# Kernel optimization log

Hardware: AMD Instinct MI355X
Metric: run time of the kernel (lower is better)

Reference implementation:

```python
import jax, jax.numpy as jnp
import numpy as np

B, S, DM1, DM2, DK, DV = 8, 2048, 768, 768, 64, 64
EPS = 1e-5


def setup_inputs() -> dict:
    key = jax.random.key(0)
    ks = jax.random.split(key, 8)
    s1 = 1.0 / np.sqrt(DM1)
    s2 = 1.0 / np.sqrt(DM2)
    return {
        "x_1": jax.random.normal(ks[0], (B, S, DM1), jnp.float32),
        "x_2": jax.random.normal(ks[1], (B, S, DM2), jnp.float32),
        "Wq": jax.random.uniform(ks[2], (DM1, DK), jnp.float32, -s1, s1),
        "bq": jnp.zeros((DK,), jnp.float32),
        "Wk": jax.random.uniform(ks[3], (DM2, DK), jnp.float32, -s2, s2),
        "bk": jnp.zeros((DK,), jnp.float32),
        "Wv": jax.random.uniform(ks[4], (DM2, DV), jnp.float32, -s2, s2),
        "bv": jnp.zeros((DV,), jnp.float32),
        "gamma": jnp.ones((DV,), jnp.float32),
        "beta": jnp.zeros((DV,), jnp.float32),
    }


def reference(x_1, x_2, Wq, bq, Wk, bk, Wv, bv, gamma, beta):
    q = jnp.einsum("bsd,dk->bsk", x_1, Wq) + bq            # [B,S,DK]
    k = jnp.einsum("bsd,dk->bsk", x_2, Wk) + bk            # [B,S,DK]
    v = jnp.einsum("bsd,dv->bsv", x_2, Wv) + bv            # [B,S,DV]
    scores = jnp.einsum("bqk,bsk->bqs", q, k) / jnp.sqrt(jnp.float32(DK))
    w = jax.nn.softmax(scores, axis=-1)                    # [B,S,S]
    # reverse-weight transform (reverse=True)
    dim = w.shape[1]
    w = (1.0 - w) / (dim - 1)
    attn = jnp.einsum("bqs,bsv->bqv", w, v)                # [B,S,DV]
    mu = jnp.mean(attn, axis=-1, keepdims=True)
    var = jnp.var(attn, axis=-1, keepdims=True)
    out = (attn - mu) * jax.lax.rsqrt(var + EPS) * gamma + beta
    return out
```

## Files before the change

### kernel.cpp

```cpp
#include <hip/hip_runtime.h>
#include <hip/hip_bf16.h>

#define BATCH 8
#define SEQ   2048
#define DM    768
#define DD    64
#define BS (BATCH * SEQ)
#define SCALEQ 0.1803369380478f

typedef __bf16 bf16x8 __attribute__((ext_vector_type(8)));
typedef float  f32x4  __attribute__((ext_vector_type(4)));
typedef short  short8 __attribute__((ext_vector_type(8)));
typedef short  short4v __attribute__((ext_vector_type(4)));

#define MFMA16(a, b, c) __builtin_amdgcn_mfma_f32_16x16x32_bf16((a), (b), (c), 0, 0, 0)

__device__ __forceinline__ short f2bf(float x) {
    unsigned u = __builtin_bit_cast(unsigned, x);
    u = (u + 0x7fffu + ((u >> 16) & 1u)) >> 16;
    return (short)u;
}
__device__ __forceinline__ float bf2f(short s) {
    unsigned u = ((unsigned)(unsigned short)s) << 16;
    return __builtin_bit_cast(float, u);
}
__device__ __forceinline__ bf16x8 cvt8(float4 a, float4 b) {
    bf16x8 r;
    r[0] = (__bf16)a.x; r[1] = (__bf16)a.y; r[2] = (__bf16)a.z; r[3] = (__bf16)a.w;
    r[4] = (__bf16)b.x; r[5] = (__bf16)b.y; r[6] = (__bf16)b.z; r[7] = (__bf16)b.w;
    return r;
}

__global__ void prep_w_kernel(const float* __restrict__ Wq, const float* __restrict__ Wk,
                              const float* __restrict__ Wv, short* __restrict__ Wt,
                              float* __restrict__ C) {
    int idx = blockIdx.x * 256 + threadIdx.x;
    if (idx < BATCH * DD) C[idx] = 0.f;
    if (idx >= 3 * DM * DD) return;
    int m = idx / (DM * DD);
    int r = (idx % (DM * DD)) / DD;
    int c = idx % DD;
    const float* W = (m == 0) ? Wq : (m == 1) ? Wk : Wv;
    float scale = (m == 0) ? SCALEQ : 1.0f;
    Wt[m * DM * DD + c * DM + r] = f2bf(W[r * DD + c] * scale);
}

__global__ __launch_bounds__(256, 2) void proj_kernel(
        const float* __restrict__ x1, const float* __restrict__ x2,
        const short* __restrict__ Wt,
        const float* __restrict__ bq, const float* __restrict__ bk,
        const float* __restrict__ bv,
        short* __restrict__ Qs, short* __restrict__ Kb, short* __restrict__ Vtb,
        float* __restrict__ C) {
    const int tid = threadIdx.x, wave = tid >> 6, lane = tid & 63;
    const int quad = lane >> 4, l15 = lane & 15;
    const int typ = blockIdx.x % 3;
    const int g   = blockIdx.x / 3;
    const int r0  = g * 64;
    const float* x = (typ == 0) ? x1 : x2;
    const int col = wave * 16 + l15;

    const short* wp = Wt + ((size_t)typ * DD + col) * DM + quad * 8;
    bf16x8 wreg[24];
#pragma unroll
    for (int st = 0; st < 24; st++)
        wreg[st] = *(const bf16x8*)(wp + st * 32);

    const float* xp = x + (size_t)(r0 + l15) * DM + quad * 8;

    f32x4 acc[4] = {};
    float4 ca[4], cb[4];
#pragma unroll
    for (int rn = 0; rn < 4; rn++) {
        const float* p = xp + (size_t)(rn * 16) * DM;
        ca[rn] = *(const float4*)(p);
        cb[rn] = *(const float4*)(p + 4);
    }
#pragma unroll
    for (int st = 0; st < 24; st++) {
        float4 na[4], nb[4];
        if (st + 1 < 24) {
#pragma unroll
            for (int rn = 0; rn < 4; rn++) {
                const float* p = xp + (size_t)(rn * 16) * DM + (st + 1) * 32;
                na[rn] = *(const float4*)(p);
                nb[rn] = *(const float4*)(p + 4);
            }
        }
#pragma unroll
        for (int rn = 0; rn < 4; rn++) {
            bf16x8 af = cvt8(ca[rn], cb[rn]);
            acc[rn] = MFMA16(af, wreg[st], acc[rn]);
        }
#pragma unroll
        for (int rn = 0; rn < 4; rn++) { ca[rn] = na[rn]; cb[rn] = nb[rn]; }
    }

    if (typ == 0) {
        float bb = bq[col] * SCALEQ;
#pragma unroll
        for (int rn = 0; rn < 4; rn++)
#pragma unroll
            for (int r = 0; r < 4; r++)
                Qs[(size_t)(r0 + rn * 16 + quad * 4 + r) * DD + col] = f2bf(acc[rn][r] + bb);
    } else if (typ == 1) {
        float bb = bk[col];
#pragma unroll
        for (int rn = 0; rn < 4; rn++)
#pragma unroll
            for (int r = 0; r < 4; r++)
                Kb[(size_t)(r0 + rn * 16 + quad * 4 + r) * DD + col] = f2bf(acc[rn][r] + bb);
    } else {
        const int b  = r0 >> 11;
        const int sb = r0 & 2047;
        float bb = bv[col];
        short* vout = Vtb + ((size_t)b * DD + col) * SEQ + sb;
        float cs = 0.f;
#pragma unroll
        for (int rn = 0; rn < 4; rn++) {
            short4v pk;
#pragma unroll
            for (int r = 0; r < 4; r++) {
                pk[r] = f2bf(acc[rn][r] + bb);
                cs += bf2f(pk[r]);
            }
            *(short4v*)(vout + rn * 16 + quad * 4) = pk;
        }
        cs += __shfl_xor(cs, 16);
        cs += __shfl_xor(cs, 32);
        if (quad == 0) atomicAdd(&C[b * DD + col], cs);
    }
}

#define PBS 72
__global__ __launch_bounds__(256, 2) void flash_kernel(
        const short* __restrict__ Q, const short* __restrict__ K,
        const short* __restrict__ Vt,
        short* __restrict__ Yp, float* __restrict__ Dp) {
    __shared__ __align__(16) short pbuf[4][64 * PBS];
    __shared__ float dl[4][64];
    const int tid  = threadIdx.x;
    const int wave = tid >> 6, lane = tid & 63, quad = lane >> 4, l15 = lane & 15;
    const int blk = blockIdx.x;
    const int b = blk & 7, qt = (blk >> 3) & 31, half = blk >> 8;
    const int q0 = qt * 64;

    bf16x8 qf[4][2];
#pragma unroll
    for (int qn = 0; qn < 4; qn++)
#pragma unroll
        for (int kc = 0; kc < 2; kc++)
            qf[qn][kc] = *(const bf16x8*)(Q + ((size_t)(b * SEQ + q0 + qn * 16 + l15)) * DD
                                          + kc * 32 + quad * 8);

    const short* Kbp = K  + (size_t)b * SEQ * DD;
    const short* Vbp = Vt + (size_t)b * DD * SEQ;
    f32x4 y[4][4] = {};
    float den[4] = {0.f, 0.f, 0.f, 0.f};
    short* pw = &pbuf[wave][0];

    const int s_begin = half * 1024 + wave * 256;
    for (int s0 = s_begin; s0 < s_begin + 256; s0 += 64) {
#pragma unroll
        for (int tn = 0; tn < 4; tn++) {
            const short* kf = Kbp + (size_t)(s0 + tn * 16 + l15) * DD + quad * 8;
            bf16x8 ka0 = *(const bf16x8*)kf;
            bf16x8 ka1 = *(const bf16x8*)(kf + 32);
#pragma unroll
            for (int qn = 0; qn < 4; qn++) {
                f32x4 z = {0.f, 0.f, 0.f, 0.f};
                z = MFMA16(ka0, qf[qn][0], z);
                z = MFMA16(ka1, qf[qn][1], z);
                short4v pk;
#pragma unroll
                for (int r = 0; r < 4; r++) {
                    float p = __builtin_amdgcn_exp2f(z[r]);
                    den[qn] += p;
                    pk[r] = f2bf(p);
                }
                *(short4v*)&pw[(qn * 16 + l15) * PBS + tn * 16 + quad * 4] = pk;
            }
        }
#pragma unroll
        for (int kc = 0; kc < 2; kc++) {
            bf16x8 pB[4];
#pragma unroll
            for (int qn = 0; qn < 4; qn++)
                pB[qn] = *(const bf16x8*)&pw[(qn * 16 + l15) * PBS + kc * 32 + quad * 8];
#pragma unroll
            for (int vn = 0; vn < 4; vn++) {
                bf16x8 va = *(const bf16x8*)(Vbp + (size_t)(vn * 16 + l15) * SEQ
                                             + s0 + kc * 32 + quad * 8);
#pragma unroll
                for (int qn = 0; qn < 4; qn++)
                    y[qn][vn] = MFMA16(va, pB[qn], y[qn][vn]);
            }
        }
    }
#pragma unroll
    for (int qn = 0; qn < 4; qn++) {
        den[qn] += __shfl_xor(den[qn], 16);
        den[qn] += __shfl_xor(den[qn], 32);
    }
#pragma unroll
    for (int qn = 0; qn < 4; qn++) {
#pragma unroll
        for (int vn = 0; vn < 4; vn++) {
            short4v pk;
#pragma unroll
            for (int r = 0; r < 4; r++) pk[r] = f2bf(y[qn][vn][r]);
            *(short4v*)&pw[(qn * 16 + l15) * PBS + vn * 16 + quad * 4] = pk;
        }
        if (quad == 0) dl[wave][qn * 16 + l15] = den[qn];
    }
    __syncthreads();
    {
        const int q = wave * 16 + l15;
        float D = dl[0][q] + dl[1][q] + dl[2][q] + dl[3][q];
        float ys[16];
#pragma unroll
        for (int j = 0; j < 16; j++) ys[j] = 0.f;
#pragma unroll
        for (int u = 0; u < 4; u++) {
#pragma unroll
            for (int h = 0; h < 2; h++) {
                bf16x8 t = *(const bf16x8*)&pbuf[u][q * PBS + quad * 16 + h * 8];
#pragma unroll
                for (int j = 0; j < 8; j++) ys[h * 8 + j] += (float)t[j];
            }
        }
        const size_t row = (size_t)b * SEQ + q0 + q;
        short8 o0, o1;
#pragma unroll
        for (int j = 0; j < 8; j++) { o0[j] = f2bf(ys[j]); o1[j] = f2bf(ys[8 + j]); }
        short* yout = Yp + ((size_t)half * BS + row) * DD + quad * 16;
        *(short8*)yout = o0;
        *(short8*)(yout + 8) = o1;
        if (quad == 0) Dp[half * BS + row] = D;
    }
}

__global__ __launch_bounds__(256) void reduce_ln_kernel(
        const short* __restrict__ Yp, const float* __restrict__ Dp,
        const float* __restrict__ C, const float* __restrict__ gamma,
        const float* __restrict__ beta, float* __restrict__ out) {
    const int row = blockIdx.x * 4 + (threadIdx.x >> 6);
    const int v = threadIdx.x & 63;
    const int b = row >> 11;
    float Y = bf2f(Yp[(size_t)row * DD + v]) + bf2f(Yp[((size_t)BS + row) * DD + v]);
    float D = Dp[row] + Dp[BS + row];
    float attn = (C[b * DD + v] - Y / D) * (1.0f / (float)(SEQ - 1));
    float msum = attn, ssum = attn * attn;
#pragma unroll
    for (int m = 1; m < 64; m <<= 1) {
        msum += __shfl_xor(msum, m);
        ssum += __shfl_xor(ssum, m);
    }
    float mu = msum * (1.0f / 64.0f);
    float var = ssum * (1.0f / 64.0f) - mu * mu;
    float rs = rsqrtf(var + 1e-5f);
    out[(size_t)row * DD + v] = (attn - mu) * rs * gamma[v] + beta[v];
}

extern "C" void kernel_launch(void* const* d_in, const int* in_sizes, int n_in,
                              void* d_out, int out_size, void* d_ws, size_t ws_size,
                              hipStream_t stream) {
    const float* x1    = (const float*)d_in[0];
    const float* x2    = (const float*)d_in[1];
    const float* Wq    = (const float*)d_in[2];
    const float* bq    = (const float*)d_in[3];
    const float* Wk    = (const float*)d_in[4];
    const float* bk    = (const float*)d_in[5];
    const float* Wv    = (const float*)d_in[6];
    const float* bv    = (const float*)d_in[7];
    const float* gamma = (const float*)d_in[8];
    const float* beta  = (const float*)d_in[9];
    float* out = (float*)d_out;

    char* ws = (char*)d_ws;
    short* Qs  = (short*)(ws);
    short* Kbf = (short*)(ws + (2ull << 20));
    short* Vtb = (short*)(ws + (4ull << 20));
    short* Wt  = (short*)(ws + (6ull << 20));
    float* Cc  = (float*)(ws + (6ull << 20) + 3 * DM * DD * 2);
    short* Yp  = (short*)(ws + (7ull << 20));
    float* Dp  = (float*)(ws + (11ull << 20));

    prep_w_kernel<<<576, 256, 0, stream>>>(Wq, Wk, Wv, Wt, Cc);
    proj_kernel<<<768, 256, 0, stream>>>(x1, x2, Wt, bq, bk, bv, Qs, Kbf, Vtb, Cc);
    flash_kernel<<<512, 256, 0, stream>>>(Qs, Kbf, Vtb, Yp, Dp);
    reduce_ln_kernel<<<BS / 4, 256, 0, stream>>>(Yp, Dp, Cc, gamma, beta, out);
}
```

Measured before the change: 212.6 us.

## Stage projection weights through double-buffered LDS via global_load_lds

The projection kernel no longer keeps all 24 weight fragments in registers per lane. It streams the weights in four phases into a double-buffered shared-memory tile using direct global-to-LDS loads, and raises the launch bound from 2 to 3 blocks per CU. The aim is to cut register pressure and raise occupancy so the memory-bound streaming of x hides latency better. In exchange it adds LDS reads and a block barrier per phase, and correctness relies on the async LDS loads having completed before each barrier.

Result: slower. 219.5 us (+3.2%).

```diff
diff --git a/kernel.cpp b/kernel.cpp
--- a/kernel.cpp
+++ b/kernel.cpp
@@ -29,6 +29,11 @@
     r[0] = (__bf16)a.x; r[1] = (__bf16)a.y; r[2] = (__bf16)a.z; r[3] = (__bf16)a.w;
     r[4] = (__bf16)b.x; r[5] = (__bf16)b.y; r[6] = (__bf16)b.z; r[7] = (__bf16)b.w;
     return r;
+}
+__device__ __forceinline__ void gload_lds16(const short* g, short* l) {
+    __builtin_amdgcn_global_load_lds(
+        (const __attribute__((address_space(1))) void*)g,
+        (__attribute__((address_space(3))) void*)l, 16, 0, 0);
 }
 
 __global__ void prep_w_kernel(const float* __restrict__ Wq, const float* __restrict__ Wk,
@@ -45,13 +50,25 @@
     Wt[m * DM * DD + c * DM + r] = f2bf(W[r * DD + c] * scale);
 }
 
-__global__ __launch_bounds__(256, 2) void proj_kernel(
+#define PHK  192
+#define SEGS 24
+__device__ __forceinline__ void stage_phase(short* dst, const short* wsrc_lane,
+                                            int p, int wave) {
+#pragma unroll
+    for (int i = 0; i < 6; i++) {
+        int s = wave * 6 + i;
+        gload_lds16(wsrc_lane + p * PHK + s * 8, dst + s * 512);
+    }
+}
+
+__global__ __launch_bounds__(256, 3) void proj_kernel(
         const float* __restrict__ x1, const float* __restrict__ x2,
         const short* __restrict__ Wt,
         const float* __restrict__ bq, const float* __restrict__ bk,
         const float* __restrict__ bv,
         short* __restrict__ Qs, short* __restrict__ Kb, short* __restrict__ Vtb,
         float* __restrict__ C) {
+    __shared__ __align__(16) short wls[2][SEGS * 512];
     const int tid = threadIdx.x, wave = tid >> 6, lane = tid & 63;
     const int quad = lane >> 4, l15 = lane & 15;
     const int typ = blockIdx.x % 3;
@@ -60,11 +77,7 @@
     const float* x = (typ == 0) ? x1 : x2;
     const int col = wave * 16 + l15;
 
-    const short* wp = Wt + ((size_t)typ * DD + col) * DM + quad * 8;
-    bf16x8 wreg[24];
-#pragma unroll
-    for (int st = 0; st < 24; st++)
-        wreg[st] = *(const bf16x8*)(wp + st * 32);
+    const short* wsrc = Wt + (size_t)(typ * DD + lane) * DM;
 
     const float* xp = x + (size_t)(r0 + l15) * DM + quad * 8;
 
@@ -76,24 +89,35 @@
         ca[rn] = *(const float4*)(p);
         cb[rn] = *(const float4*)(p + 4);
     }
-#pragma unroll
-    for (int st = 0; st < 24; st++) {
-        float4 na[4], nb[4];
-        if (st + 1 < 24) {
+
+    stage_phase(&wls[0][0], wsrc, 0, wave);
+    __syncthreads();
+
+#pragma unroll
+    for (int p = 0; p < 4; p++) {
+        if (p + 1 < 4) stage_phase(&wls[(p + 1) & 1][0], wsrc, p + 1, wave);
+#pragma unroll
+        for (int st6 = 0; st6 < 6; st6++) {
+            const int st = p * 6 + st6;
+            float4 na[4], nb[4];
+            if (st + 1 < 24) {
+#pragma unroll
+                for (int rn = 0; rn < 4; rn++) {
+                    const float* ptr = xp + (size_t)(rn * 16) * DM + (st + 1) * 32;
+                    na[rn] = *(const float4*)(ptr);
+                    nb[rn] = *(const float4*)(ptr + 4);
+                }
+            }
+            bf16x8 wf = *(const bf16x8*)&wls[p & 1][(st6 * 4 + quad) * 512 + col * 8];
 #pragma unroll
             for (int rn = 0; rn < 4; rn++) {
-                const float* p = xp + (size_t)(rn * 16) * DM + (st + 1) * 32;
-                na[rn] = *(const float4*)(p);
-                nb[rn] = *(const float4*)(p + 4);
-            }
-        }
-#pragma unroll
-        for (int rn = 0; rn < 4; rn++) {
-            bf16x8 af = cvt8(ca[rn], cb[rn]);
-            acc[rn] = MFMA16(af, wreg[st], acc[rn]);
-        }
-#pragma unroll
-        for (int rn = 0; rn < 4; rn++) { ca[rn] = na[rn]; cb[rn] = nb[rn]; }
+                bf16x8 af = cvt8(ca[rn], cb[rn]);
+                acc[rn] = MFMA16(af, wf, acc[rn]);
+            }
+#pragma unroll
+            for (int rn = 0; rn < 4; rn++) { ca[rn] = na[rn]; cb[rn] = nb[rn]; }
+        }
+        __syncthreads();
     }
 
     if (typ == 0) {
```
